# Kernel tuning notes

Hardware: AMD Instinct MI355X
Metric: run time of the kernel (lower is better)

## Reference

```python
import jax, jax.numpy as jnp
import numpy as np

KERNEL_SIZE = 128


def _thumbnail(img, k):
    # Non-overlapping box average: [B,C,H,W] -> [B,C,H//k,W//k]
    B, C, H, W = img.shape
    x = img.reshape(B, C, H // k, k, W // k, k)
    return x.mean(axis=(3, 5))


def setup_inputs() -> dict:
    key = jax.random.key(0)
    k1, k2 = jax.random.split(key)
    shape = (32, 1, 1024, 1024)
    fake_img = jax.random.normal(k1, shape, dtype=jnp.float32)
    real_img = jax.random.normal(k2, shape, dtype=jnp.float32)
    return {"fake_img": fake_img, "real_img": real_img}


def reference(fake_img, real_img):
    k = KERNEL_SIZE
    real_t = _thumbnail(real_img, k)
    fake_t = _thumbnail(fake_img, k)
    # L1 norm over (C, h, w) per sample, then mean over batch
    per_sample = jnp.sum(jnp.abs(fake_t - real_t), axis=(1, 2, 3))
    return per_sample.mean()
```

## Files before the change

kernel.cpp:

```cpp
#include <hip/hip_runtime.h>


__global__ __launch_bounds__(256) void thumb_l1_kernel(
    const float* __restrict__ fake,
    const float* __restrict__ real,
    float* __restrict__ out)
{
    const int bid = blockIdx.x;
    const int tid = threadIdx.x;

    const int b  = bid >> 6;
    const int ci = bid & 63;
    const int cy = ci >> 3;
    const int cx = ci & 7;

    const size_t base = (size_t)b * (1024u * 1024u)
                      + (size_t)cy * (128u * 1024u)
                      + (size_t)cx * 128u;

    const float4* __restrict__ f4 = (const float4*)(fake + base);
    const float4* __restrict__ r4 = (const float4*)(real + base);

    const int row0 = tid >> 5;
    const int c4   = tid & 31;

    float acc = 0.0f;
#pragma unroll
    for (int p = 0; p < 16; ++p) {
        const int row = (p << 3) + row0;
        const size_t idx = (size_t)row * 256 + c4;
        const float4 f = f4[idx];
        const float4 r = r4[idx];
        acc += (f.x - r.x) + (f.y - r.y) + (f.z - r.z) + (f.w - r.w);
    }

    #pragma unroll
    for (int off = 32; off > 0; off >>= 1)
        acc += __shfl_down(acc, off, 64);

    __shared__ float wsum[4];
    const int wave = tid >> 6;
    if ((tid & 63) == 0) wsum[wave] = acc;
    __syncthreads();

    if (tid == 0) {
        const float s = wsum[0] + wsum[1] + wsum[2] + wsum[3];
        atomicAdd(out, fabsf(s) * (1.0f / (16384.0f * 32.0f)));
    }
}

extern "C" void kernel_launch(void* const* d_in, const int* in_sizes, int n_in,
                              void* d_out, int out_size, void* d_ws, size_t ws_size,
                              hipStream_t stream) {
    const float* fake = (const float*)d_in[0];
    const float* real = (const float*)d_in[1];
    float* out = (float*)d_out;

    hipMemsetAsync(out, 0, sizeof(float), stream);

    thumb_l1_kernel<<<2048, 256, 0, stream>>>(fake, real, out);
}
```

Baseline: 284.7 us.

## Split into row-contiguous partial-sum pass and single-block cell-gather reduction

```diff
diff --git a/kernel.cpp b/kernel.cpp
--- a/kernel.cpp
+++ b/kernel.cpp
@@ -1,52 +1,63 @@
 #include <hip/hip_runtime.h>
 
 
-__global__ __launch_bounds__(256) void thumb_l1_kernel(
+#define ROWS_PER_BLOCK 16
+#define N_STAGE1_BLOCKS 2048
+
+__global__ __launch_bounds__(256) void thumb_stage1(
     const float* __restrict__ fake,
     const float* __restrict__ real,
-    float* __restrict__ out)
+    float* __restrict__ partial)
 {
     const int bid = blockIdx.x;
     const int tid = threadIdx.x;
 
-    const int b  = bid >> 6;
-    const int ci = bid & 63;
-    const int cy = ci >> 3;
-    const int cx = ci & 7;
-
-    const size_t base = (size_t)b * (1024u * 1024u)
-                      + (size_t)cy * (128u * 1024u)
-                      + (size_t)cx * 128u;
-
-    const float4* __restrict__ f4 = (const float4*)(fake + base);
-    const float4* __restrict__ r4 = (const float4*)(real + base);
-
-    const int row0 = tid >> 5;
-    const int c4   = tid & 31;
+    const size_t base = (size_t)bid * ROWS_PER_BLOCK * 256 + tid;
+    const float4* __restrict__ f4 = (const float4*)fake + base;
+    const float4* __restrict__ r4 = (const float4*)real + base;
 
     float acc = 0.0f;
-#pragma unroll
-    for (int p = 0; p < 16; ++p) {
-        const int row = (p << 3) + row0;
-        const size_t idx = (size_t)row * 256 + c4;
-        const float4 f = f4[idx];
-        const float4 r = r4[idx];
-        acc += (f.x - r.x) + (f.y - r.y) + (f.z - r.z) + (f.w - r.w);
+#pragma unroll 4
+    for (int r = 0; r < ROWS_PER_BLOCK; ++r) {
+        const float4 f = f4[(size_t)r * 256];
+        const float4 g = r4[(size_t)r * 256];
+        acc += (f.x - g.x) + (f.y - g.y) + (f.z - g.z) + (f.w - g.w);
     }
 
-    #pragma unroll
+#pragma unroll
+    for (int off = 16; off > 0; off >>= 1)
+        acc += __shfl_down(acc, off, 32);
+
+    if ((tid & 31) == 0)
+        partial[(size_t)bid * 8 + (tid >> 5)] = acc;
+}
+
+__global__ __launch_bounds__(256) void thumb_stage2(
+    const float* __restrict__ partial,
+    float* __restrict__ out)
+{
+    const int tid = threadIdx.x;
+
+    float acc = 0.0f;
+    for (int c = tid; c < 2048; c += 256) {
+        const int base = (c >> 3) * 64 + (c & 7);
+        float s = 0.0f;
+#pragma unroll
+        for (int g = 0; g < 8; ++g)
+            s += partial[base + g * 8];
+        acc += fabsf(s);
+    }
+
+#pragma unroll
     for (int off = 32; off > 0; off >>= 1)
         acc += __shfl_down(acc, off, 64);
 
     __shared__ float wsum[4];
-    const int wave = tid >> 6;
-    if ((tid & 63) == 0) wsum[wave] = acc;
+    if ((tid & 63) == 0) wsum[tid >> 6] = acc;
     __syncthreads();
 
-    if (tid == 0) {
-        const float s = wsum[0] + wsum[1] + wsum[2] + wsum[3];
-        atomicAdd(out, fabsf(s) * (1.0f / (16384.0f * 32.0f)));
-    }
+    if (tid == 0)
+        out[0] = (wsum[0] + wsum[1] + wsum[2] + wsum[3]) * (1.0f / (16384.0f * 32.0f));
 }
 
 extern "C" void kernel_launch(void* const* d_in, const int* in_sizes, int n_in,
@@ -55,8 +66,8 @@
     const float* fake = (const float*)d_in[0];
     const float* real = (const float*)d_in[1];
     float* out = (float*)d_out;
+    float* partial = (float*)d_ws;
 
-    hipMemsetAsync(out, 0, sizeof(float), stream);
-
-    thumb_l1_kernel<<<2048, 256, 0, stream>>>(fake, real, out);
+    thumb_stage1<<<N_STAGE1_BLOCKS, 256, 0, stream>>>(fake, real, partial);
+    thumb_stage2<<<1, 256, 0, stream>>>(partial, out);
 }
```

Measured after the change: 278.9 us. -2.0%, faster.
